# Kernel optimization log

Hardware: AMD Instinct MI355X
Metric: run time of the kernel (lower is better)

Reference implementation:

```python
import jax, jax.numpy as jnp
import numpy as np

EPS = 1e-5  # torch BatchNorm default eps
B_SEG = 64
PTS_PER_SEG = 16384
N_TOTAL = B_SEG * PTS_PER_SEG
D_IN = 32
D_OUT = 64


def setup_inputs() -> dict:
    key = jax.random.key(0)
    k = jax.random.split(key, 4)
    x = jax.random.normal(k[0], (N_TOTAL, D_IN), dtype=jnp.float32)
    length = jnp.full((B_SEG,), PTS_PER_SEG, dtype=jnp.int32)
    # conv1d_1: Conv1d(32, 1, 1) -> weight [1,32,1], bias [1]; flatten to vector/scalar
    w1 = jax.random.normal(k[1], (D_IN,), dtype=jnp.float32) * 0.1
    b1 = jnp.zeros((), dtype=jnp.float32)
    # bn_1: BatchNorm1d(1)
    g1 = jnp.ones((), dtype=jnp.float32)
    beta1 = jnp.zeros((), dtype=jnp.float32)
    # fc_1: Linear(32, 64)
    W2 = jax.random.normal(k[2], (D_IN, D_OUT), dtype=jnp.float32) * 0.05
    b2 = jnp.zeros((D_OUT,), dtype=jnp.float32)
    # bn_2: BatchNorm1d(64)
    g2 = jnp.ones((D_OUT,), dtype=jnp.float32)
    beta2 = jnp.zeros((D_OUT,), dtype=jnp.float32)
    return {"x": x, "length": length, "w1": w1, "b1": b1, "g1": g1,
            "beta1": beta1, "W2": W2, "b2": b2, "g2": g2, "beta2": beta2}


def reference(x, length, w1, b1, g1, beta1, W2, b2, g2, beta2):
    N = x.shape[0]
    B = length.shape[0]
    # conv1d(32->1, k=1) over all N points: per-point scalar score
    z = x @ w1 + b1                                        # [N]
    # BatchNorm1d(1) in training mode: stats over all N points (biased var)
    mu = jnp.mean(z)
    var = jnp.var(z)
    out1 = g1 * (z - mu) * jax.lax.rsqrt(var + EPS) + beta1  # [N]

    # segment ids from ragged lengths (total length is static)
    seg = jnp.repeat(jnp.arange(B, dtype=jnp.int32), length,
                     total_repeat_length=N)                 # [N]

    # sft = mean(x * out1[:,None], axis=1), softmax per segment
    s = jnp.mean(x * out1[:, None], axis=1)                 # [N]
    smax = jax.ops.segment_max(s, seg, num_segments=B)      # [B]
    e = jnp.exp(s - smax[seg])                              # [N]
    denom = jax.ops.segment_sum(e, seg, num_segments=B)     # [B]
    w = e / denom[seg]                                      # [N] softmax weights

    # temp = mean over segment of (x * w)  (mean, not weighted sum)
    pooled = jax.ops.segment_sum(x * w[:, None], seg, num_segments=B)
    pooled = pooled / length[:, None].astype(x.dtype)       # [B, 32]

    # fc + BatchNorm1d(64) in training mode (stats over B rows)
    h = pooled @ W2 + b2                                    # [B, 64]
    mu2 = jnp.mean(h, axis=0)
    var2 = jnp.var(h, axis=0)
    out = g2 * (h - mu2) * jax.lax.rsqrt(var2 + EPS) + beta2
    return out
```

## Files before the change

### kernel.cpp

```cpp
#include <hip/hip_runtime.h>


#define EPS 1e-5f
#define NSB 1024
#define CHUNKS 16

#define WS_DPART   0
#define WS_CONSTS  16384
#define WS_OFFS    16416
#define WS_GNUM    16896
#define WS_GDEN    25088

__global__ __launch_bounds__(256, 4) void k_stats(const float* __restrict__ x,
                                                  const float* __restrict__ w1,
                                                  const float* __restrict__ b1,
                                                  int N,
                                                  double* __restrict__ dpart) {
    const int tid = threadIdx.x;
    const float b1v = b1[0];
    const float4* __restrict__ xv = (const float4*)x;

    const int stride = gridDim.x * 256;
    double accZ = 0.0, accZZ = 0.0;

    for (int row = blockIdx.x * 256 + tid; row < N; row += stride) {
        const float4* __restrict__ rp = xv + (size_t)row * 8;
        float4 v[8];
#pragma unroll
        for (int i = 0; i < 8; ++i) v[i] = rp[i];
        float z = b1v;
#pragma unroll
        for (int i = 0; i < 8; ++i) {
            z = fmaf(v[i].x, w1[4 * i + 0], z);
            z = fmaf(v[i].y, w1[4 * i + 1], z);
            z = fmaf(v[i].z, w1[4 * i + 2], z);
            z = fmaf(v[i].w, w1[4 * i + 3], z);
        }
        accZ  += (double)z;
        accZZ += (double)z * (double)z;
    }

    __shared__ double sZ[256], sZZ[256];
    sZ[tid] = accZ; sZZ[tid] = accZZ;
    __syncthreads();
    for (int s = 128; s > 0; s >>= 1) {
        if (tid < s) { sZ[tid] += sZ[tid + s]; sZZ[tid] += sZZ[tid + s]; }
        __syncthreads();
    }
    if (tid == 0) {
        dpart[2 * blockIdx.x]     = sZ[0];
        dpart[2 * blockIdx.x + 1] = sZZ[0];
    }
}

__global__ __launch_bounds__(256) void k_consts(const double* __restrict__ dpart,
                                                const int* __restrict__ length,
                                                const float* __restrict__ g1,
                                                const float* __restrict__ beta1,
                                                int N, int B,
                                                float* __restrict__ consts,
                                                int* __restrict__ offs,
                                                float* __restrict__ gnum,
                                                float* __restrict__ gden) {
    __shared__ double sZ[256], sZZ[256];
    const int tid = threadIdx.x;

    for (int i = tid; i < B * 32; i += 256) gnum[i] = 0.f;
    if (tid < B) gden[tid] = 0.f;

    double aZ = 0.0, aZZ = 0.0;
    for (int i = tid; i < NSB; i += 256) {
        aZ  += dpart[2 * i];
        aZZ += dpart[2 * i + 1];
    }
    sZ[tid] = aZ; sZZ[tid] = aZZ;
    __syncthreads();
    for (int s = 128; s > 0; s >>= 1) {
        if (tid < s) { sZ[tid] += sZ[tid + s]; sZZ[tid] += sZZ[tid + s]; }
        __syncthreads();
    }
    if (tid == 0) {
        double mu  = sZ[0] / (double)N;
        double var = sZZ[0] / (double)N - mu * mu;
        float c1 = (float)((double)g1[0] / sqrt(var + (double)EPS));
        float c2 = beta1[0] - (float)(c1 * mu);
        consts[0] = c1;
        consts[1] = c2;
        int o = 0;
        offs[0] = 0;
        for (int b = 0; b < B; ++b) { o += length[b]; offs[b + 1] = o; }
    }
}

__global__ __launch_bounds__(256, 4) void k_pool(const float* __restrict__ x,
                                                 const float* __restrict__ w1,
                                                 const float* __restrict__ b1,
                                                 const float* __restrict__ consts,
                                                 const int* __restrict__ offs,
                                                 float* __restrict__ gnum,
                                                 float* __restrict__ gden) {
    const int tid = threadIdx.x;
    const int b = blockIdx.y;
    const int off = offs[b];
    const int len = offs[b + 1] - off;
    const int rpc = (len + CHUNKS - 1) / CHUNKS;
    const int r0 = blockIdx.x * rpc;
    const int r1 = min(r0 + rpc, len);

    const float b1v = b1[0];
    const float c1 = consts[0], c2 = consts[1];
    const float4* __restrict__ xv = (const float4*)x;

    float4 acc[8];
#pragma unroll
    for (int i = 0; i < 8; ++i) acc[i] = make_float4(0.f, 0.f, 0.f, 0.f);
    float accE = 0.f;

    for (int r = r0 + tid; r < r1; r += 256) {
        const float4* __restrict__ rp = xv + (size_t)(off + r) * 8;
        float4 v[8];
#pragma unroll
        for (int i = 0; i < 8; ++i) v[i] = rp[i];
        float z = b1v, m = 0.f;
#pragma unroll
        for (int i = 0; i < 8; ++i) {
            z = fmaf(v[i].x, w1[4 * i + 0], z);
            z = fmaf(v[i].y, w1[4 * i + 1], z);
            z = fmaf(v[i].z, w1[4 * i + 2], z);
            z = fmaf(v[i].w, w1[4 * i + 3], z);
            m += v[i].x + v[i].y + v[i].z + v[i].w;
        }
        float s = (c1 * z + c2) * m * 0.03125f;
        float e = __expf(s);
#pragma unroll
        for (int i = 0; i < 8; ++i) {
            acc[i].x = fmaf(e, v[i].x, acc[i].x);
            acc[i].y = fmaf(e, v[i].y, acc[i].y);
            acc[i].z = fmaf(e, v[i].z, acc[i].z);
            acc[i].w = fmaf(e, v[i].w, acc[i].w);
        }
        accE += e;
    }

#pragma unroll
    for (int msk = 1; msk < 64; msk <<= 1) {
#pragma unroll
        for (int i = 0; i < 8; ++i) {
            acc[i].x += __shfl_xor(acc[i].x, msk);
            acc[i].y += __shfl_xor(acc[i].y, msk);
            acc[i].z += __shfl_xor(acc[i].z, msk);
            acc[i].w += __shfl_xor(acc[i].w, msk);
        }
        accE += __shfl_xor(accE, msk);
    }

    __shared__ float sred[4][33];
    const int wave = tid >> 6;
    const int lane = tid & 63;
    if (lane == 0) {
#pragma unroll
        for (int i = 0; i < 8; ++i) {
            sred[wave][4 * i + 0] = acc[i].x;
            sred[wave][4 * i + 1] = acc[i].y;
            sred[wave][4 * i + 2] = acc[i].z;
            sred[wave][4 * i + 3] = acc[i].w;
        }
        sred[wave][32] = accE;
    }
    __syncthreads();
    if (tid < 33) {
        float s = sred[0][tid] + sred[1][tid] + sred[2][tid] + sred[3][tid];
        if (tid < 32) atomicAdd(&gnum[b * 32 + tid], s);
        else          atomicAdd(&gden[b], s);
    }
}

__global__ __launch_bounds__(256) void k_head(const float* __restrict__ gnum,
                                              const float* __restrict__ gden,
                                              const int* __restrict__ length,
                                              const float* __restrict__ W2,
                                              const float* __restrict__ b2,
                                              const float* __restrict__ g2,
                                              const float* __restrict__ beta2,
                                              float* __restrict__ out, int B) {
    __shared__ float pooled[64 * 32];
    __shared__ float h[64 * 64];
    __shared__ float mu2[64], isd[64];
    const int tid = threadIdx.x;

    for (int i = tid; i < B * 32; i += 256) {
        int bb = i >> 5;
        pooled[i] = gnum[i] / (gden[bb] * (float)length[bb]);
    }
    __syncthreads();

    const int j = tid & 63;
    const int g = tid >> 6;
    for (int r = 0; r < 16; ++r) {
        int bb = g * 16 + r;
        if (bb < B) {
            float hv = b2[j];
            for (int k = 0; k < 32; ++k) hv += pooled[bb * 32 + k] * W2[k * 64 + j];
            h[bb * 64 + j] = hv;
        }
    }
    __syncthreads();

    if (tid < 64) {
        float m = 0.f;
        for (int bb = 0; bb < B; ++bb) m += h[bb * 64 + tid];
        m /= (float)B;
        float v = 0.f;
        for (int bb = 0; bb < B; ++bb) { float d = h[bb * 64 + tid] - m; v += d * d; }
        v /= (float)B;
        mu2[tid] = m;
        isd[tid] = rsqrtf(v + EPS);
    }
    __syncthreads();

    for (int r = 0; r < 16; ++r) {
        int bb = g * 16 + r;
        if (bb < B) {
            int idx = bb * 64 + j;
            out[idx] = g2[j] * (h[idx] - mu2[j]) * isd[j] + beta2[j];
        }
    }
}

extern "C" void kernel_launch(void* const* d_in, const int* in_sizes, int n_in,
                              void* d_out, int out_size, void* d_ws, size_t ws_size,
                              hipStream_t stream) {
    const float* x      = (const float*)d_in[0];
    const int*   length = (const int*)  d_in[1];
    const float* w1     = (const float*)d_in[2];
    const float* b1     = (const float*)d_in[3];
    const float* g1     = (const float*)d_in[4];
    const float* beta1  = (const float*)d_in[5];
    const float* W2     = (const float*)d_in[6];
    const float* b2     = (const float*)d_in[7];
    const float* g2     = (const float*)d_in[8];
    const float* beta2  = (const float*)d_in[9];
    float* out = (float*)d_out;

    const int N = in_sizes[0] / 32;
    const int B = in_sizes[1];

    char* ws = (char*)d_ws;
    double* dpart  = (double*)(ws + WS_DPART);
    float*  consts = (float*) (ws + WS_CONSTS);
    int*    offs   = (int*)   (ws + WS_OFFS);
    float*  gnum   = (float*) (ws + WS_GNUM);
    float*  gden   = (float*) (ws + WS_GDEN);

    k_stats <<<NSB, 256, 0, stream>>>(x, w1, b1, N, dpart);
    k_consts<<<1,   256, 0, stream>>>(dpart, length, g1, beta1, N, B,
                                      consts, offs, gnum, gden);
    k_pool  <<<dim3(CHUNKS, B), 256, 0, stream>>>(x, w1, b1, consts, offs, gnum, gden);
    k_head  <<<1,   256, 0, stream>>>(gnum, gden, length, W2, b2, g2, beta2, out, B);
}
```

Measured before the change: 250.0 us.

## Fuse consts and head kernels into stats/pool via last-block reduction

Cuts the four-kernel pipeline down to two. The accumulator zeroing moves into k_stats. Each k_pool block now redundantly reduces the 1024 stats partials and computes its own segment offset. The head (fc plus BatchNorm) runs in whichever pool block arrives last on an atomic counter. This removes two tiny single-block launches and their serialization gaps, at the cost of repeated partial reductions in every pool block, larger shared memory per block, and a serial tail in the last block.

```diff
diff --git a/kernel.cpp b/kernel.cpp
--- a/kernel.cpp
+++ b/kernel.cpp
@@ -6,23 +6,30 @@
 #define CHUNKS 16
 
 #define WS_DPART   0
-#define WS_CONSTS  16384
-#define WS_OFFS    16416
-#define WS_GNUM    16896
-#define WS_GDEN    25088
+#define WS_GNUM    16384
+#define WS_GDEN    24576
+#define WS_CNT     24832
 
 __global__ __launch_bounds__(256, 4) void k_stats(const float* __restrict__ x,
                                                   const float* __restrict__ w1,
                                                   const float* __restrict__ b1,
-                                                  int N,
-                                                  double* __restrict__ dpart) {
+                                                  int N, int B,
+                                                  double* __restrict__ dpart,
+                                                  float* __restrict__ gnum,
+                                                  float* __restrict__ gden,
+                                                  unsigned int* __restrict__ cnt) {
     const int tid = threadIdx.x;
+    if (blockIdx.x == 0) {
+        for (int i = tid; i < B * 32; i += 256) gnum[i] = 0.f;
+        if (tid < B) gden[tid] = 0.f;
+        if (tid == 0) *cnt = 0u;
+    }
+
     const float b1v = b1[0];
     const float4* __restrict__ xv = (const float4*)x;
-
     const int stride = gridDim.x * 256;
+
     double accZ = 0.0, accZZ = 0.0;
-
     for (int row = blockIdx.x * 256 + tid; row < N; row += stride) {
         const float4* __restrict__ rp = xv + (size_t)row * 8;
         float4 v[8];
@@ -53,62 +60,66 @@
     }
 }
 
-__global__ __launch_bounds__(256) void k_consts(const double* __restrict__ dpart,
-                                                const int* __restrict__ length,
-                                                const float* __restrict__ g1,
-                                                const float* __restrict__ beta1,
-                                                int N, int B,
-                                                float* __restrict__ consts,
-                                                int* __restrict__ offs,
-                                                float* __restrict__ gnum,
-                                                float* __restrict__ gden) {
-    __shared__ double sZ[256], sZZ[256];
-    const int tid = threadIdx.x;
-
-    for (int i = tid; i < B * 32; i += 256) gnum[i] = 0.f;
-    if (tid < B) gden[tid] = 0.f;
-
-    double aZ = 0.0, aZZ = 0.0;
-    for (int i = tid; i < NSB; i += 256) {
-        aZ  += dpart[2 * i];
-        aZZ += dpart[2 * i + 1];
-    }
-    sZ[tid] = aZ; sZZ[tid] = aZZ;
-    __syncthreads();
-    for (int s = 128; s > 0; s >>= 1) {
-        if (tid < s) { sZ[tid] += sZ[tid + s]; sZZ[tid] += sZZ[tid + s]; }
-        __syncthreads();
-    }
-    if (tid == 0) {
-        double mu  = sZ[0] / (double)N;
-        double var = sZZ[0] / (double)N - mu * mu;
-        float c1 = (float)((double)g1[0] / sqrt(var + (double)EPS));
-        float c2 = beta1[0] - (float)(c1 * mu);
-        consts[0] = c1;
-        consts[1] = c2;
-        int o = 0;
-        offs[0] = 0;
-        for (int b = 0; b < B; ++b) { o += length[b]; offs[b + 1] = o; }
-    }
-}
-
 __global__ __launch_bounds__(256, 4) void k_pool(const float* __restrict__ x,
+                                                 const int* __restrict__ length,
                                                  const float* __restrict__ w1,
                                                  const float* __restrict__ b1,
-                                                 const float* __restrict__ consts,
-                                                 const int* __restrict__ offs,
+                                                 const float* __restrict__ g1,
+                                                 const float* __restrict__ beta1,
+                                                 const float* __restrict__ W2,
+                                                 const float* __restrict__ b2,
+                                                 const float* __restrict__ g2,
+                                                 const float* __restrict__ beta2,
+                                                 float* __restrict__ out,
+                                                 int N, int B,
+                                                 const double* __restrict__ dpart,
                                                  float* __restrict__ gnum,
-                                                 float* __restrict__ gden) {
+                                                 float* __restrict__ gden,
+                                                 unsigned int* __restrict__ cnt) {
     const int tid = threadIdx.x;
-    const int b = blockIdx.y;
-    const int off = offs[b];
-    const int len = offs[b + 1] - off;
+    const int c = blockIdx.x, b = blockIdx.y;
+    const int nblk = gridDim.x * gridDim.y;
+
+    __shared__ double sZ[256], sZZ[256];
+    __shared__ float sc[2];
+    __shared__ float sred[4][33];
+    __shared__ int sseg[2];
+
+    if (tid == 0) {
+        int o = 0;
+        for (int i = 0; i < b; ++i) o += length[i];
+        sseg[0] = o; sseg[1] = length[b];
+    }
+
+    {
+        double aZ = 0.0, aZZ = 0.0;
+#pragma unroll
+        for (int k = 0; k < NSB / 256; ++k) {
+            int i = k * 256 + tid;
+            aZ  += dpart[2 * i];
+            aZZ += dpart[2 * i + 1];
+        }
+        sZ[tid] = aZ; sZZ[tid] = aZZ;
+        __syncthreads();
+        for (int s = 128; s > 0; s >>= 1) {
+            if (tid < s) { sZ[tid] += sZ[tid + s]; sZZ[tid] += sZZ[tid + s]; }
+            __syncthreads();
+        }
+        if (tid == 0) {
+            double mu  = sZ[0] / (double)N;
+            double var = sZZ[0] / (double)N - mu * mu;
+            float c1 = (float)((double)g1[0] / sqrt(var + (double)EPS));
+            sc[0] = c1;
+            sc[1] = beta1[0] - (float)(c1 * mu);
+        }
+        __syncthreads();
+    }
+    const float c1 = sc[0], c2 = sc[1];
+    const int off = sseg[0], len = sseg[1];
     const int rpc = (len + CHUNKS - 1) / CHUNKS;
-    const int r0 = blockIdx.x * rpc;
-    const int r1 = min(r0 + rpc, len);
+    const int r0 = c * rpc, r1 = min(r0 + rpc, len);
 
     const float b1v = b1[0];
-    const float c1 = consts[0], c2 = consts[1];
     const float4* __restrict__ xv = (const float4*)x;
 
     float4 acc[8];
@@ -153,8 +164,6 @@
         }
         accE += __shfl_xor(accE, msk);
     }
-
-    __shared__ float sred[4][33];
     const int wave = tid >> 6;
     const int lane = tid & 63;
     if (lane == 0) {
@@ -173,24 +182,24 @@
         if (tid < 32) atomicAdd(&gnum[b * 32 + tid], s);
         else          atomicAdd(&gden[b], s);
     }
-}
-
-__global__ __launch_bounds__(256) void k_head(const float* __restrict__ gnum,
-                                              const float* __restrict__ gden,
-                                              const int* __restrict__ length,
-                                              const float* __restrict__ W2,
-                                              const float* __restrict__ b2,
-                                              const float* __restrict__ g2,
-                                              const float* __restrict__ beta2,
-                                              float* __restrict__ out, int B) {
+
+    __threadfence();
+    __shared__ unsigned int sold;
+    __syncthreads();
+    if (tid == 0) sold = atomicAdd(cnt, 1u);
+    __syncthreads();
+    if (sold != (unsigned int)(nblk - 1)) return;
+    __threadfence();
+
     __shared__ float pooled[64 * 32];
-    __shared__ float h[64 * 64];
+    __shared__ float hmat[64 * 64];
     __shared__ float mu2[64], isd[64];
-    const int tid = threadIdx.x;
 
     for (int i = tid; i < B * 32; i += 256) {
         int bb = i >> 5;
-        pooled[i] = gnum[i] / (gden[bb] * (float)length[bb]);
+        float num = atomicAdd(&gnum[i], 0.f);
+        float den = atomicAdd(&gden[bb], 0.f);
+        pooled[i] = num / (den * (float)length[bb]);
     }
     __syncthreads();
 
@@ -200,18 +209,19 @@
         int bb = g * 16 + r;
         if (bb < B) {
             float hv = b2[j];
-            for (int k = 0; k < 32; ++k) hv += pooled[bb * 32 + k] * W2[k * 64 + j];
-            h[bb * 64 + j] = hv;
+            for (int k = 0; k < 32; ++k)
+                hv += pooled[bb * 32 + k] * W2[k * 64 + j];
+            hmat[bb * 64 + j] = hv;
         }
     }
     __syncthreads();
 
     if (tid < 64) {
         float m = 0.f;
-        for (int bb = 0; bb < B; ++bb) m += h[bb * 64 + tid];
+        for (int bb = 0; bb < B; ++bb) m += hmat[bb * 64 + tid];
         m /= (float)B;
         float v = 0.f;
-        for (int bb = 0; bb < B; ++bb) { float d = h[bb * 64 + tid] - m; v += d * d; }
+        for (int bb = 0; bb < B; ++bb) { float d = hmat[bb * 64 + tid] - m; v += d * d; }
         v /= (float)B;
         mu2[tid] = m;
         isd[tid] = rsqrtf(v + EPS);
@@ -222,7 +232,7 @@
         int bb = g * 16 + r;
         if (bb < B) {
             int idx = bb * 64 + j;
-            out[idx] = g2[j] * (h[idx] - mu2[j]) * isd[j] + beta2[j];
+            out[idx] = g2[j] * (hmat[idx] - mu2[j]) * isd[j] + beta2[j];
         }
     }
 }
@@ -246,15 +256,13 @@
     const int B = in_sizes[1];
 
     char* ws = (char*)d_ws;
-    double* dpart  = (double*)(ws + WS_DPART);
-    float*  consts = (float*) (ws + WS_CONSTS);
-    int*    offs   = (int*)   (ws + WS_OFFS);
-    float*  gnum   = (float*) (ws + WS_GNUM);
-    float*  gden   = (float*) (ws + WS_GDEN);
-
-    k_stats <<<NSB, 256, 0, stream>>>(x, w1, b1, N, dpart);
-    k_consts<<<1,   256, 0, stream>>>(dpart, length, g1, beta1, N, B,
-                                      consts, offs, gnum, gden);
-    k_pool  <<<dim3(CHUNKS, B), 256, 0, stream>>>(x, w1, b1, consts, offs, gnum, gden);
-    k_head  <<<1,   256, 0, stream>>>(gnum, gden, length, W2, b2, g2, beta2, out, B);
+    double*       dpart = (double*)      (ws + WS_DPART);
+    float*        gnum  = (float*)       (ws + WS_GNUM);
+    float*        gden  = (float*)       (ws + WS_GDEN);
+    unsigned int* cnt   = (unsigned int*)(ws + WS_CNT);
+
+    k_stats<<<NSB, 256, 0, stream>>>(x, w1, b1, N, B, dpart, gnum, gden, cnt);
+    k_pool <<<dim3(CHUNKS, B), 256, 0, stream>>>(x, length, w1, b1, g1, beta1,
+                                                 W2, b2, g2, beta2, out, N, B,
+                                                 dpart, gnum, gden, cnt);
 }
```

Result: slower. 355.4 us (+42.2%).
